# Performance work log

Measured on AMD Instinct MI355X. Metric: run time of the kernel, lower is better.

Reference implementation:

```python
import jax, jax.numpy as jnp
import numpy as np

N, DIM, QK, HEADS, NWIN, TOPK = 1, 128, 128, 8, 8, 4
D = H = W = 32


def setup_inputs() -> dict:
    key = jax.random.key(0)
    ks = jax.random.split(key, 3)
    s = lambda fan: 1.0 / np.sqrt(fan)
    return {
        "x": jax.random.normal(ks[0], (N, D, H, W, DIM), jnp.float32),
        "w_qkv": jax.random.normal(ks[1], (DIM, 2 * QK + DIM), jnp.float32) * s(DIM),
        "b_qkv": jnp.zeros((2 * QK + DIM,), jnp.float32),
        "w_o": jax.random.normal(ks[2], (DIM, DIM), jnp.float32) * s(DIM),
        "b_o": jnp.zeros((DIM,), jnp.float32),
    }


def _forward(x, w_qkv, b_qkv, w_o, b_o):
    n, Dd, Hh, Ww, C = x.shape
    d, h, w = Dd // NWIN, Hh // NWIN, Ww // NWIN
    p3, w3 = NWIN ** 3, d * h * w
    cq, cv = QK // HEADS, DIM // HEADS
    scale = QK ** -0.5
    # window partition: n (q d)(j h)(i w) c -> n (q j i) d h w c
    xw = x.reshape(n, NWIN, d, NWIN, h, NWIN, w, C)
    xw = xw.transpose(0, 1, 3, 5, 2, 4, 6, 7).reshape(n, p3, d, h, w, C)
    # fused qkv projection
    qkv = xw @ w_qkv + b_qkv
    q, k, v = qkv[..., :QK], qkv[..., QK:2 * QK], qkv[..., 2 * QK:]
    q_pix = q.reshape(n, p3, w3, QK)
    kv_pix = jnp.concatenate([k, v], axis=-1).reshape(n, p3, w3, QK + DIM)
    # region-level routing (non-differentiable: detached in original)
    q_win = jax.lax.stop_gradient(q.mean((2, 3, 4)))  # (n, p3, QK)
    k_win = jax.lax.stop_gradient(k.mean((2, 3, 4)))
    logits = jnp.einsum('npc,nqc->npq', q_win * scale, k_win)  # (n, p3, p3)
    _, r_idx = jax.lax.top_k(logits, TOPK)  # (n, p3, topk)
    # gather top-k regions' KV per query window: (n, p3, topk, w3, QK+DIM)
    kv_sel = jax.vmap(lambda kvp, idx: kvp[idx])(kv_pix, r_idx)
    k_sel = kv_sel[..., :QK].reshape(n * p3, TOPK * w3, HEADS, cq).transpose(0, 2, 3, 1)  # (np3, m, cq, k*w3)
    v_sel = kv_sel[..., QK:].reshape(n * p3, TOPK * w3, HEADS, cv).transpose(0, 2, 1, 3)  # (np3, m, k*w3, cv)
    qh = q_pix.reshape(n * p3, w3, HEADS, cq).transpose(0, 2, 1, 3)  # (np3, m, w3, cq)
    attn = jax.nn.softmax((qh * scale) @ k_sel, axis=-1)  # (np3, m, w3, k*w3)
    out = attn @ v_sel  # (np3, m, w3, cv)
    # (n q j i) m (d h w) c -> n (q d)(j h)(i w)(m c)
    out = out.reshape(n, NWIN, NWIN, NWIN, HEADS, d, h, w, cv)
    out = out.transpose(0, 1, 5, 2, 6, 3, 7, 4, 8).reshape(n, Dd, Hh, Ww, DIM)
    out = out @ w_o + b_o
    return out, q, k, v


def reference(x, w_qkv, b_qkv, w_o, b_o):
    return _forward(x, w_qkv, b_qkv, w_o, b_o)
```

## Files before the change

### kernel.cpp

```cpp
#include <hip/hip_runtime.h>
#include <cmath>

namespace {

typedef __attribute__((ext_vector_type(8))) short short8;
typedef __attribute__((ext_vector_type(4))) float f32x4;
typedef __attribute__((ext_vector_type(4))) unsigned u32x4;

constexpr float kScale = 0.08838834764831845f;

__device__ __forceinline__ int voxel_row(int p, int pix) {
  int pd = p >> 6, ph = (p >> 3) & 7, pw = p & 7;
  int iz = pix >> 4, iy = (pix >> 2) & 3, ix = pix & 3;
  return (((pd * 4 + iz) * 32 + (ph * 4 + iy)) * 32 + (pw * 4 + ix));
}

__device__ __forceinline__ float dot4(float4 a, float4 b) {
  return a.x * b.x + a.y * b.y + a.z * b.z + a.w * b.w;
}

__device__ __forceinline__ short bf16c(float f) {
  unsigned u = __builtin_bit_cast(unsigned, f);
  u += 0x7fffu + ((u >> 16) & 1u);
  return (short)(u >> 16);
}

__device__ __forceinline__ unsigned bfpack(float lo, float hi) {
  return (unsigned)(unsigned short)bf16c(lo) |
         ((unsigned)(unsigned short)bf16c(hi) << 16);
}

__device__ __forceinline__ short8 cvt8(const float* src) {
  float4 a = *(const float4*)src, b = *(const float4*)(src + 4);
  short8 o;
  o[0] = bf16c(a.x); o[1] = bf16c(a.y); o[2] = bf16c(a.z); o[3] = bf16c(a.w);
  o[4] = bf16c(b.x); o[5] = bf16c(b.y); o[6] = bf16c(b.z); o[7] = bf16c(b.w);
  return o;
}

__global__ __launch_bounds__(64) void k_pack2(
    const float* __restrict__ wqkv, const float* __restrict__ wo,
    short* __restrict__ dstq, short* __restrict__ dsto) {
  const int lane = threadIdx.x;
  const float* w;
  short* dst;
  int fid, N;
  if (blockIdx.x < 96) {
    w = wqkv; dst = dstq; fid = blockIdx.x; N = 384;
  } else {
    w = wo; dst = dsto; fid = blockIdx.x - 96; N = 128;
  }
  const int ntile = fid >> 2, ks = fid & 3;
  const int k0 = ks * 32 + (lane >> 4) * 8, col = ntile * 16 + (lane & 15);
  short8 o;
#pragma unroll
  for (int i = 0; i < 8; ++i) o[i] = bf16c(w[(size_t)(k0 + i) * N + col]);
  *(short8*)(dst + ((size_t)fid * 64 + lane) * 8) = o;
}

__global__ __launch_bounds__(256) void k_qkv(
    const float* __restrict__ x, const short* __restrict__ wpk,
    const float* __restrict__ bias, const float* __restrict__ wfull,
    float* __restrict__ q, float* __restrict__ k, float* __restrict__ v,
    short* __restrict__ vt, short* __restrict__ kbh, short* __restrict__ qbh,
    float* __restrict__ qwin, float* __restrict__ kwin) {
  __shared__ short sX[64][136];
  __shared__ float xpart[16][16][8];
  __shared__ float xm[128];
  const int p = blockIdx.x, t = threadIdx.x;
  const int wave = t >> 6, lane = t & 63, l15 = lane & 15, lg = lane >> 4;

  float ps[8] = {0.f, 0.f, 0.f, 0.f, 0.f, 0.f, 0.f, 0.f};
#pragma unroll
  for (int r = 0; r < 4; ++r) {
    int unit = t + r * 256;
    int row = unit >> 4, u = unit & 15;
    const float* src = x + (size_t)voxel_row(p, row) * 128 + u * 8;
    float4 a = *(const float4*)src, b = *(const float4*)(src + 4);
    ps[0] += a.x; ps[1] += a.y; ps[2] += a.z; ps[3] += a.w;
    ps[4] += b.x; ps[5] += b.y; ps[6] += b.z; ps[7] += b.w;
    short8 o;
    o[0] = bf16c(a.x); o[1] = bf16c(a.y); o[2] = bf16c(a.z); o[3] = bf16c(a.w);
    o[4] = bf16c(b.x); o[5] = bf16c(b.y); o[6] = bf16c(b.z); o[7] = bf16c(b.w);
    *(short8*)(&sX[row][u * 8]) = o;
  }
#pragma unroll
  for (int i = 0; i < 8; ++i) xpart[t >> 4][t & 15][i] = ps[i];
  __syncthreads();
  if (t < 128) {
    float s = 0.f;
#pragma unroll
    for (int g = 0; g < 16; ++g) s += xpart[g][t >> 3][t & 7];
    xm[t] = s * (1.f / 64.f);
  }
  __syncthreads();

  f32x4 acc[4][6];
#pragma unroll
  for (int mt = 0; mt < 4; ++mt)
#pragma unroll
    for (int nt = 0; nt < 6; ++nt) acc[mt][nt] = f32x4{0.f, 0.f, 0.f, 0.f};
#pragma unroll
  for (int ks = 0; ks < 4; ++ks) {
    short8 a[4];
#pragma unroll
    for (int mt = 0; mt < 4; ++mt)
      a[mt] = *(const short8*)(&sX[mt * 16 + l15][ks * 32 + lg * 8]);
#pragma unroll
    for (int nt = 0; nt < 6; ++nt) {
      int ntg = wave * 6 + nt;
      short8 b = *(const short8*)(wpk + ((size_t)(ntg * 4 + ks) * 64 + lane) * 8);
#pragma unroll
      for (int mt = 0; mt < 4; ++mt)
        acc[mt][nt] = __builtin_amdgcn_mfma_f32_16x16x32_bf16(a[mt], b, acc[mt][nt], 0, 0, 0);
    }
  }
#pragma unroll
  for (int nt = 0; nt < 6; ++nt) {
    int n = (wave * 6 + nt) * 16 + l15;
    float bv = bias[n];
    float* dst = n < 128 ? q : (n < 256 ? k : v);
    int col = n & 127;
#pragma unroll
    for (int mt = 0; mt < 4; ++mt) {
      float o0 = acc[mt][nt][0] + bv, o1 = acc[mt][nt][1] + bv;
      float o2 = acc[mt][nt][2] + bv, o3 = acc[mt][nt][3] + bv;
      int row0 = mt * 16 + lg * 4;
      dst[(size_t)(p * 64 + row0 + 0) * 128 + col] = o0;
      dst[(size_t)(p * 64 + row0 + 1) * 128 + col] = o1;
      dst[(size_t)(p * 64 + row0 + 2) * 128 + col] = o2;
      dst[(size_t)(p * 64 + row0 + 3) * 128 + col] = o3;
      if (n >= 256) {
        uint2 pk;
        pk.x = bfpack(o0, o1);
        pk.y = bfpack(o2, o3);
        *(uint2*)(vt + (size_t)p * 8192 + (size_t)(n - 256) * 64 + row0) = pk;
      } else if (n >= 128) {
        int hh = (n - 128) >> 4, d = (n - 128) & 15;
        short* kd = kbh + (((size_t)(p * 8 + hh)) * 64 + row0) * 16 + d;
        kd[0] = bf16c(o0);
        kd[16] = bf16c(o1);
        kd[32] = bf16c(o2);
        kd[48] = bf16c(o3);
      } else {
        int hh = n >> 4, d = n & 15;
        short* qd = qbh + (((size_t)(p * 8 + hh)) * 64 + row0) * 16 + d;
        qd[0] = bf16c(o0 * kScale);
        qd[16] = bf16c(o1 * kScale);
        qd[32] = bf16c(o2 * kScale);
        qd[48] = bf16c(o3 * kScale);
      }
    }
  }

  {
    float acc2 = bias[t];
    for (int kk = 0; kk < 128; ++kk)
      acc2 = fmaf(xm[kk], wfull[(size_t)kk * 384 + t], acc2);
    if (t < 128) qwin[p * 128 + t] = acc2;
    else kwin[p * 128 + (t - 128)] = acc2;
  }
}

__global__ __launch_bounds__(256) void k_route(
    const float* __restrict__ qwin, const float* __restrict__ kwin,
    int* __restrict__ ridx) {
  __shared__ float qs[128];
  __shared__ float lg[512];
  __shared__ float rv[256];
  __shared__ int ri[256];
  const int p = blockIdx.x, t = threadIdx.x;
  if (t < 32) *(float4*)(&qs[t * 4]) = *(const float4*)(qwin + p * 128 + t * 4);
  __syncthreads();
  for (int jj = t; jj < 512; jj += 256) {
    const float* kr = kwin + (size_t)jj * 128;
    float s = 0.f;
    for (int c = 0; c < 128; c += 4) {
      float4 k4 = *(const float4*)(kr + c);
      float4 q4 = *(const float4*)(qs + c);
      s += dot4(q4, k4);
    }
    lg[jj] = s;
  }
  __syncthreads();
  for (int sel = 0; sel < 4; ++sel) {
    float bv = lg[t];
    int bi = t;
    float v2 = lg[t + 256];
    if (v2 > bv) { bv = v2; bi = t + 256; }
    rv[t] = bv; ri[t] = bi;
    __syncthreads();
    for (int off = 128; off > 0; off >>= 1) {
      if (t < off && rv[t + off] > rv[t]) { rv[t] = rv[t + off]; ri[t] = ri[t + off]; }
      __syncthreads();
    }
    if (t == 0) { ridx[p * 4 + sel] = ri[0]; lg[ri[0]] = -INFINITY; }
    __syncthreads();
  }
}

__global__ __launch_bounds__(512, 4) void k_attn(
    const short* __restrict__ qbh, const short* __restrict__ kbh,
    const short* __restrict__ vt, const int* __restrict__ ridx,
    short* __restrict__ aob) {
  const int p = blockIdx.x, t = threadIdx.x;
  const int h = t >> 6, lane = t & 63;
  const int l15 = lane & 15, lg = lane >> 4;

  const int4 ws4 = *(const int4*)(ridx + p * 4);
  const int wsa[4] = {ws4.x, ws4.y, ws4.z, ws4.w};

  const int src0 = ((lg & 1) << 5) | l15;
  const int src1 = src0 + 16;

  const short* qw = qbh + ((size_t)(p * 8 + h)) * 1024;
  short8 qf[4];
#pragma unroll
  for (int nt = 0; nt < 4; ++nt) {
    if (lg < 2)
      qf[nt] = *(const short8*)(qw + (nt * 16 + l15) * 16 + lg * 8);
    else
      qf[nt] = short8{0, 0, 0, 0, 0, 0, 0, 0};
  }

  float m_r[4] = {-1e30f, -1e30f, -1e30f, -1e30f};
  float l_r[4] = {0.f, 0.f, 0.f, 0.f};
  f32x4 oacc[4];
#pragma unroll
  for (int i = 0; i < 4; ++i) oacc[i] = f32x4{0.f, 0.f, 0.f, 0.f};

#pragma unroll
  for (int c = 0; c < 4; ++c) {
    const int wsel = wsa[c];
    const short* kw = kbh + ((size_t)(wsel * 8 + h)) * 1024;
    short8 af[4];
#pragma unroll
    for (int mt = 0; mt < 4; ++mt) {
      if (lg < 2)
        af[mt] = *(const short8*)(kw + (mt * 16 + l15) * 16 + lg * 8);
      else
        af[mt] = short8{0, 0, 0, 0, 0, 0, 0, 0};
    }
    const short* vw = vt + (size_t)wsel * 8192 + (size_t)(h * 16 + l15) * 64 + lg * 8;
    short8 av0 = *(const short8*)(vw);
    short8 av1 = *(const short8*)(vw + 32);

#pragma unroll
    for (int nt = 0; nt < 4; ++nt) {
      f32x4 s[4];
#pragma unroll
      for (int mt = 0; mt < 4; ++mt)
        s[mt] = __builtin_amdgcn_mfma_f32_16x16x32_bf16(
            af[mt], qf[nt], f32x4{0.f, 0.f, 0.f, 0.f}, 0, 0, 0);
      float mx = -1e30f;
#pragma unroll
      for (int mt = 0; mt < 4; ++mt)
#pragma unroll
        for (int j = 0; j < 4; ++j) mx = fmaxf(mx, s[mt][j]);
      mx = fmaxf(mx, __shfl_xor(mx, 16));
      mx = fmaxf(mx, __shfl_xor(mx, 32));
      float mnew = fmaxf(m_r[nt], mx);
      float sc = __expf(m_r[nt] - mnew);
      m_r[nt] = mnew;
      float ls = 0.f;
#pragma unroll
      for (int mt = 0; mt < 4; ++mt)
#pragma unroll
        for (int j = 0; j < 4; ++j) {
          float e = __expf(s[mt][j] - mnew);
          s[mt][j] = e;
          ls += e;
        }
      ls += __shfl_xor(ls, 16);
      ls += __shfl_xor(ls, 32);
      l_r[nt] = l_r[nt] * sc + ls;
      oacc[nt][0] *= sc; oacc[nt][1] *= sc;
      oacc[nt][2] *= sc; oacc[nt][3] *= sc;
      unsigned P2[4][2];
#pragma unroll
      for (int mt = 0; mt < 4; ++mt) {
        P2[mt][0] = bfpack(s[mt][0], s[mt][1]);
        P2[mt][1] = bfpack(s[mt][2], s[mt][3]);
      }
#pragma unroll
      for (int kt = 0; kt < 2; ++kt) {
        unsigned lo0 = (unsigned)__shfl((int)P2[2 * kt + 0][0], src0);
        unsigned hi0 = (unsigned)__shfl((int)P2[2 * kt + 1][0], src0);
        unsigned lo1 = (unsigned)__shfl((int)P2[2 * kt + 0][1], src0);
        unsigned hi1 = (unsigned)__shfl((int)P2[2 * kt + 1][1], src0);
        unsigned lo2 = (unsigned)__shfl((int)P2[2 * kt + 0][0], src1);
        unsigned hi2 = (unsigned)__shfl((int)P2[2 * kt + 1][0], src1);
        unsigned lo3 = (unsigned)__shfl((int)P2[2 * kt + 0][1], src1);
        unsigned hi3 = (unsigned)__shfl((int)P2[2 * kt + 1][1], src1);
        u32x4 bw;
        bw[0] = (lg < 2) ? lo0 : hi0;
        bw[1] = (lg < 2) ? lo1 : hi1;
        bw[2] = (lg < 2) ? lo2 : hi2;
        bw[3] = (lg < 2) ? lo3 : hi3;
        short8 bfr = __builtin_bit_cast(short8, bw);
        oacc[nt] = __builtin_amdgcn_mfma_f32_16x16x32_bf16(
            kt == 0 ? av0 : av1, bfr, oacc[nt], 0, 0, 0);
      }
    }
  }

#pragma unroll
  for (int nt = 0; nt < 4; ++nt) {
    float inv = 1.f / l_r[nt];
    uint2 pk;
    pk.x = bfpack(oacc[nt][0] * inv, oacc[nt][1] * inv);
    pk.y = bfpack(oacc[nt][2] * inv, oacc[nt][3] * inv);
    int qpix = nt * 16 + l15;
    *(uint2*)(aob + ((size_t)(p * 64 + qpix)) * 128 + h * 16 + lg * 4) = pk;
  }
}

__global__ __launch_bounds__(256) void k_proj(
    const short* __restrict__ aob, const short* __restrict__ wpk,
    const float* __restrict__ bias, float* __restrict__ out) {
  const int p = blockIdx.x, t = threadIdx.x;
  const int wave = t >> 6, lane = t & 63, l15 = lane & 15, lg = lane >> 4;
  f32x4 acc[4][2];
#pragma unroll
  for (int mt = 0; mt < 4; ++mt) {
    acc[mt][0] = f32x4{0.f, 0.f, 0.f, 0.f};
    acc[mt][1] = f32x4{0.f, 0.f, 0.f, 0.f};
  }
#pragma unroll
  for (int ks = 0; ks < 4; ++ks) {
    short8 a[4];
#pragma unroll
    for (int mt = 0; mt < 4; ++mt)
      a[mt] = *(const short8*)(aob + ((size_t)(p * 64 + mt * 16 + l15)) * 128 + ks * 32 + lg * 8);
#pragma unroll
    for (int nt = 0; nt < 2; ++nt) {
      int ntg = wave * 2 + nt;
      short8 b = *(const short8*)(wpk + ((size_t)(ntg * 4 + ks) * 64 + lane) * 8);
#pragma unroll
      for (int mt = 0; mt < 4; ++mt)
        acc[mt][nt] = __builtin_amdgcn_mfma_f32_16x16x32_bf16(a[mt], b, acc[mt][nt], 0, 0, 0);
    }
  }
#pragma unroll
  for (int nt = 0; nt < 2; ++nt) {
    int n = (wave * 2 + nt) * 16 + l15;
    float bv = bias[n];
#pragma unroll
    for (int mt = 0; mt < 4; ++mt)
#pragma unroll
      for (int j = 0; j < 4; ++j)
        out[(size_t)voxel_row(p, mt * 16 + lg * 4 + j) * 128 + n] = acc[mt][nt][j] + bv;
  }
}

}

extern "C" void kernel_launch(void* const* d_in, const int* in_sizes, int n_in,
                              void* d_out, int out_size, void* d_ws, size_t ws_size,
                              hipStream_t stream) {
  (void)in_sizes; (void)n_in; (void)out_size; (void)ws_size;
  const float* x = (const float*)d_in[0];
  const float* w_qkv = (const float*)d_in[1];
  const float* b_qkv = (const float*)d_in[2];
  const float* w_o = (const float*)d_in[3];
  const float* b_o = (const float*)d_in[4];

  float* out = (float*)d_out;
  float* q = out + 4194304;
  float* k = q + 4194304;
  float* v = k + 4194304;

  float* qwin = (float*)d_ws;
  float* kwin = qwin + 65536;
  int* ridx = (int*)(kwin + 65536);
  short* wpk_qkv = (short*)(ridx + 2048);
  short* wpk_o = wpk_qkv + 49152;
  short* vt = wpk_o + 16384;
  short* kbh = vt + 4194304;
  short* qbh = kbh + 4194304;
  short* aob = qbh + 4194304;

  k_pack2<<<128, 64, 0, stream>>>(w_qkv, w_o, wpk_qkv, wpk_o);
  k_qkv<<<512, 256, 0, stream>>>(x, wpk_qkv, b_qkv, w_qkv, q, k, v, vt, kbh, qbh, qwin, kwin);
  k_route<<<512, 256, 0, stream>>>(qwin, kwin, ridx);
  k_attn<<<512, 512, 0, stream>>>(qbh, kbh, vt, ridx, aob);
  k_proj<<<512, 256, 0, stream>>>(aob, wpk_o, b_o, out);
}
```

Baseline: 87.63 us.

## Fuse routing and output projection into attention kernel; widen QKV blocks

Removes the separate routing and projection kernels. Each attention block now computes its own window logits and top-k in shared memory, then runs the output projection from a shared-memory tile, so the bf16 attention output never goes to global memory. The QKV kernel moves to 512 threads with fewer accumulator tiles per wave and does the column-sum reduction with wave shuffles. This saves two launches and a global round trip, at the cost of more serial work per attention block before the MFMA phase starts.

```diff
diff --git a/kernel.cpp b/kernel.cpp
--- a/kernel.cpp
+++ b/kernel.cpp
@@ -28,14 +28,6 @@
 __device__ __forceinline__ unsigned bfpack(float lo, float hi) {
   return (unsigned)(unsigned short)bf16c(lo) |
          ((unsigned)(unsigned short)bf16c(hi) << 16);
-}
-
-__device__ __forceinline__ short8 cvt8(const float* src) {
-  float4 a = *(const float4*)src, b = *(const float4*)(src + 4);
-  short8 o;
-  o[0] = bf16c(a.x); o[1] = bf16c(a.y); o[2] = bf16c(a.z); o[3] = bf16c(a.w);
-  o[4] = bf16c(b.x); o[5] = bf16c(b.y); o[6] = bf16c(b.z); o[7] = bf16c(b.w);
-  return o;
 }
 
 __global__ __launch_bounds__(64) void k_pack2(
@@ -58,22 +50,22 @@
   *(short8*)(dst + ((size_t)fid * 64 + lane) * 8) = o;
 }
 
-__global__ __launch_bounds__(256) void k_qkv(
+__global__ __launch_bounds__(512, 4) void k_qkv(
     const float* __restrict__ x, const short* __restrict__ wpk,
     const float* __restrict__ bias, const float* __restrict__ wfull,
     float* __restrict__ q, float* __restrict__ k, float* __restrict__ v,
     short* __restrict__ vt, short* __restrict__ kbh, short* __restrict__ qbh,
     float* __restrict__ qwin, float* __restrict__ kwin) {
   __shared__ short sX[64][136];
-  __shared__ float xpart[16][16][8];
+  __shared__ float xpart[8][16][8];
   __shared__ float xm[128];
   const int p = blockIdx.x, t = threadIdx.x;
   const int wave = t >> 6, lane = t & 63, l15 = lane & 15, lg = lane >> 4;
 
   float ps[8] = {0.f, 0.f, 0.f, 0.f, 0.f, 0.f, 0.f, 0.f};
 #pragma unroll
-  for (int r = 0; r < 4; ++r) {
-    int unit = t + r * 256;
+  for (int r = 0; r < 2; ++r) {
+    int unit = t + r * 512;
     int row = unit >> 4, u = unit & 15;
     const float* src = x + (size_t)voxel_row(p, row) * 128 + u * 8;
     float4 a = *(const float4*)src, b = *(const float4*)(src + 4);
@@ -85,21 +77,26 @@
     *(short8*)(&sX[row][u * 8]) = o;
   }
 #pragma unroll
-  for (int i = 0; i < 8; ++i) xpart[t >> 4][t & 15][i] = ps[i];
+  for (int i = 0; i < 8; ++i) {
+    ps[i] += __shfl_xor(ps[i], 16);
+    ps[i] += __shfl_xor(ps[i], 32);
+  }
+  if (lg == 0)
+#pragma unroll
+    for (int i = 0; i < 8; ++i) xpart[wave][l15][i] = ps[i];
   __syncthreads();
   if (t < 128) {
     float s = 0.f;
 #pragma unroll
-    for (int g = 0; g < 16; ++g) s += xpart[g][t >> 3][t & 7];
+    for (int w8 = 0; w8 < 8; ++w8) s += xpart[w8][t >> 3][t & 7];
     xm[t] = s * (1.f / 64.f);
   }
-  __syncthreads();
-
-  f32x4 acc[4][6];
+
+  f32x4 acc[4][3];
 #pragma unroll
   for (int mt = 0; mt < 4; ++mt)
 #pragma unroll
-    for (int nt = 0; nt < 6; ++nt) acc[mt][nt] = f32x4{0.f, 0.f, 0.f, 0.f};
+    for (int nt = 0; nt < 3; ++nt) acc[mt][nt] = f32x4{0.f, 0.f, 0.f, 0.f};
 #pragma unroll
   for (int ks = 0; ks < 4; ++ks) {
     short8 a[4];
@@ -107,8 +104,8 @@
     for (int mt = 0; mt < 4; ++mt)
       a[mt] = *(const short8*)(&sX[mt * 16 + l15][ks * 32 + lg * 8]);
 #pragma unroll
-    for (int nt = 0; nt < 6; ++nt) {
-      int ntg = wave * 6 + nt;
+    for (int nt = 0; nt < 3; ++nt) {
+      int ntg = wave * 3 + nt;
       short8 b = *(const short8*)(wpk + ((size_t)(ntg * 4 + ks) * 64 + lane) * 8);
 #pragma unroll
       for (int mt = 0; mt < 4; ++mt)
@@ -116,8 +113,8 @@
     }
   }
 #pragma unroll
-  for (int nt = 0; nt < 6; ++nt) {
-    int n = (wave * 6 + nt) * 16 + l15;
+  for (int nt = 0; nt < 3; ++nt) {
+    int n = (wave * 3 + nt) * 16 + l15;
     float bv = bias[n];
     float* dst = n < 128 ? q : (n < 256 ? k : v);
     int col = n & 127;
@@ -153,7 +150,8 @@
     }
   }
 
-  {
+  __syncthreads();
+  if (t < 256) {
     float acc2 = bias[t];
     for (int kk = 0; kk < 128; ++kk)
       acc2 = fmaf(xm[kk], wfull[(size_t)kk * 384 + t], acc2);
@@ -162,56 +160,21 @@
   }
 }
 
-__global__ __launch_bounds__(256) void k_route(
-    const float* __restrict__ qwin, const float* __restrict__ kwin,
-    int* __restrict__ ridx) {
-  __shared__ float qs[128];
-  __shared__ float lg[512];
+__global__ __launch_bounds__(512, 4) void k_attn(
+    const short* __restrict__ qbh, const short* __restrict__ kbh,
+    const short* __restrict__ vt, const float* __restrict__ qwin,
+    const float* __restrict__ kwin, const short* __restrict__ wpk_o,
+    const float* __restrict__ b_o, float* __restrict__ out) {
+  __shared__ float lgits[512];
   __shared__ float rv[256];
   __shared__ int ri[256];
-  const int p = blockIdx.x, t = threadIdx.x;
-  if (t < 32) *(float4*)(&qs[t * 4]) = *(const float4*)(qwin + p * 128 + t * 4);
-  __syncthreads();
-  for (int jj = t; jj < 512; jj += 256) {
-    const float* kr = kwin + (size_t)jj * 128;
-    float s = 0.f;
-    for (int c = 0; c < 128; c += 4) {
-      float4 k4 = *(const float4*)(kr + c);
-      float4 q4 = *(const float4*)(qs + c);
-      s += dot4(q4, k4);
-    }
-    lg[jj] = s;
-  }
-  __syncthreads();
-  for (int sel = 0; sel < 4; ++sel) {
-    float bv = lg[t];
-    int bi = t;
-    float v2 = lg[t + 256];
-    if (v2 > bv) { bv = v2; bi = t + 256; }
-    rv[t] = bv; ri[t] = bi;
-    __syncthreads();
-    for (int off = 128; off > 0; off >>= 1) {
-      if (t < off && rv[t + off] > rv[t]) { rv[t] = rv[t + off]; ri[t] = ri[t + off]; }
-      __syncthreads();
-    }
-    if (t == 0) { ridx[p * 4 + sel] = ri[0]; lg[ri[0]] = -INFINITY; }
-    __syncthreads();
-  }
-}
-
-__global__ __launch_bounds__(512, 4) void k_attn(
-    const short* __restrict__ qbh, const short* __restrict__ kbh,
-    const short* __restrict__ vt, const int* __restrict__ ridx,
-    short* __restrict__ aob) {
+  __shared__ float qs[128];
+  __shared__ int widx[4];
+  __shared__ short sO[64][136];
+
   const int p = blockIdx.x, t = threadIdx.x;
   const int h = t >> 6, lane = t & 63;
   const int l15 = lane & 15, lg = lane >> 4;
-
-  const int4 ws4 = *(const int4*)(ridx + p * 4);
-  const int wsa[4] = {ws4.x, ws4.y, ws4.z, ws4.w};
-
-  const int src0 = ((lg & 1) << 5) | l15;
-  const int src1 = src0 + 16;
 
   const short* qw = qbh + ((size_t)(p * 8 + h)) * 1024;
   short8 qf[4];
@@ -223,6 +186,36 @@
       qf[nt] = short8{0, 0, 0, 0, 0, 0, 0, 0};
   }
 
+  if (t < 32) *(float4*)(&qs[t * 4]) = *(const float4*)(qwin + p * 128 + t * 4);
+  __syncthreads();
+  {
+    const float* kr = kwin + (size_t)t * 128;
+    float s = 0.f;
+    for (int c = 0; c < 128; c += 4)
+      s += dot4(*(const float4*)(qs + c), *(const float4*)(kr + c));
+    lgits[t] = s;
+  }
+  __syncthreads();
+  for (int sel = 0; sel < 4; ++sel) {
+    if (t < 256) {
+      float bv = lgits[t];
+      int bi = t;
+      float v2 = lgits[t + 256];
+      if (v2 > bv) { bv = v2; bi = t + 256; }
+      rv[t] = bv; ri[t] = bi;
+    }
+    __syncthreads();
+    for (int off = 128; off > 0; off >>= 1) {
+      if (t < off && rv[t + off] > rv[t]) { rv[t] = rv[t + off]; ri[t] = ri[t + off]; }
+      __syncthreads();
+    }
+    if (t == 0) { widx[sel] = ri[0]; lgits[ri[0]] = -INFINITY; }
+    __syncthreads();
+  }
+
+  const int src0 = ((lg & 1) << 5) | l15;
+  const int src1 = src0 + 16;
+
   float m_r[4] = {-1e30f, -1e30f, -1e30f, -1e30f};
   float l_r[4] = {0.f, 0.f, 0.f, 0.f};
   f32x4 oacc[4];
@@ -231,7 +224,7 @@
 
 #pragma unroll
   for (int c = 0; c < 4; ++c) {
-    const int wsel = wsa[c];
+    const int wsel = widx[c];
     const short* kw = kbh + ((size_t)(wsel * 8 + h)) * 1024;
     short8 af[4];
 #pragma unroll
@@ -310,46 +303,32 @@
     uint2 pk;
     pk.x = bfpack(oacc[nt][0] * inv, oacc[nt][1] * inv);
     pk.y = bfpack(oacc[nt][2] * inv, oacc[nt][3] * inv);
-    int qpix = nt * 16 + l15;
-    *(uint2*)(aob + ((size_t)(p * 64 + qpix)) * 128 + h * 16 + lg * 4) = pk;
-  }
-}
-
-__global__ __launch_bounds__(256) void k_proj(
-    const short* __restrict__ aob, const short* __restrict__ wpk,
-    const float* __restrict__ bias, float* __restrict__ out) {
-  const int p = blockIdx.x, t = threadIdx.x;
-  const int wave = t >> 6, lane = t & 63, l15 = lane & 15, lg = lane >> 4;
-  f32x4 acc[4][2];
-#pragma unroll
-  for (int mt = 0; mt < 4; ++mt) {
-    acc[mt][0] = f32x4{0.f, 0.f, 0.f, 0.f};
-    acc[mt][1] = f32x4{0.f, 0.f, 0.f, 0.f};
-  }
+    *(uint2*)(&sO[nt * 16 + l15][h * 16 + lg * 4]) = pk;
+  }
+  __syncthreads();
+
+  f32x4 pacc[4];
+#pragma unroll
+  for (int mt = 0; mt < 4; ++mt) pacc[mt] = f32x4{0.f, 0.f, 0.f, 0.f};
 #pragma unroll
   for (int ks = 0; ks < 4; ++ks) {
     short8 a[4];
 #pragma unroll
     for (int mt = 0; mt < 4; ++mt)
-      a[mt] = *(const short8*)(aob + ((size_t)(p * 64 + mt * 16 + l15)) * 128 + ks * 32 + lg * 8);
-#pragma unroll
-    for (int nt = 0; nt < 2; ++nt) {
-      int ntg = wave * 2 + nt;
-      short8 b = *(const short8*)(wpk + ((size_t)(ntg * 4 + ks) * 64 + lane) * 8);
-#pragma unroll
-      for (int mt = 0; mt < 4; ++mt)
-        acc[mt][nt] = __builtin_amdgcn_mfma_f32_16x16x32_bf16(a[mt], b, acc[mt][nt], 0, 0, 0);
-    }
-  }
-#pragma unroll
-  for (int nt = 0; nt < 2; ++nt) {
-    int n = (wave * 2 + nt) * 16 + l15;
-    float bv = bias[n];
+      a[mt] = *(const short8*)(&sO[mt * 16 + l15][ks * 32 + lg * 8]);
+    short8 b = *(const short8*)(wpk_o + ((size_t)(h * 4 + ks) * 64 + lane) * 8);
 #pragma unroll
     for (int mt = 0; mt < 4; ++mt)
+      pacc[mt] = __builtin_amdgcn_mfma_f32_16x16x32_bf16(a[mt], b, pacc[mt], 0, 0, 0);
+  }
+  {
+    int n = h * 16 + l15;
+    float bv = b_o[n];
+#pragma unroll
+    for (int mt = 0; mt < 4; ++mt)
 #pragma unroll
       for (int j = 0; j < 4; ++j)
-        out[(size_t)voxel_row(p, mt * 16 + lg * 4 + j) * 128 + n] = acc[mt][nt][j] + bv;
+        out[(size_t)voxel_row(p, mt * 16 + lg * 4 + j) * 128 + n] = pacc[mt][j] + bv;
   }
 }
 
@@ -372,17 +351,13 @@
 
   float* qwin = (float*)d_ws;
   float* kwin = qwin + 65536;
-  int* ridx = (int*)(kwin + 65536);
-  short* wpk_qkv = (short*)(ridx + 2048);
+  short* wpk_qkv = (short*)(kwin + 65536);
   short* wpk_o = wpk_qkv + 49152;
   short* vt = wpk_o + 16384;
   short* kbh = vt + 4194304;
   short* qbh = kbh + 4194304;
-  short* aob = qbh + 4194304;
 
   k_pack2<<<128, 64, 0, stream>>>(w_qkv, w_o, wpk_qkv, wpk_o);
-  k_qkv<<<512, 256, 0, stream>>>(x, wpk_qkv, b_qkv, w_qkv, q, k, v, vt, kbh, qbh, qwin, kwin);
-  k_route<<<512, 256, 0, stream>>>(qwin, kwin, ridx);
-  k_attn<<<512, 512, 0, stream>>>(qbh, kbh, vt, ridx, aob);
-  k_proj<<<512, 256, 0, stream>>>(aob, wpk_o, b_o, out);
-}
+  k_qkv<<<512, 512, 0, stream>>>(x, wpk_qkv, b_qkv, w_qkv, q, k, v, vt, kbh, qbh, qwin, kwin);
+  k_attn<<<512, 512, 0, stream>>>(qbh, kbh, vt, qwin, kwin, wpk_o, b_o, out);
+}
```

Result: faster. 78.45 us (-10.5%).
